# Performance work log

Hardware: AMD Instinct MI355X
Metric: run time of the kernel (lower is better)

Reference implementation:

```python
import jax, jax.numpy as jnp
import numpy as np


def conv1d(x, w, b, pad):
    # x: (B, Cin, T), w: (Cout, Cin, K), b: (Cout,)
    y = jax.lax.conv_general_dilated(x, w, window_strides=(1,), padding=[(pad, pad)],
                                     dimension_numbers=('NCH', 'OIH', 'NCH'))
    return y + b[None, :, None]


def setup_inputs() -> dict:
    key = jax.random.key(0)
    ks = jax.random.split(key, 12)
    B, Cm, T1, Ct, T2, Ca = 8, 80, 800, 512, 200, 80
    queries = jax.random.normal(ks[0], (B, Cm, T1), dtype=jnp.float32)
    keys = jax.random.normal(ks[1], (B, Ct, T2), dtype=jnp.float32)
    query_lens = jnp.full((B,), T1, dtype=jnp.int32)
    key_lens = jax.random.randint(ks[2], (B,), T2 // 2, T2 + 1)
    # mask True where key position is padding (>= key_len): (B, T2, 1)
    mask = (jnp.arange(T2)[None, :] >= key_lens[:, None])[:, :, None]
    attn_prior = jax.random.uniform(ks[3], (B, T1, T2), dtype=jnp.float32) + 0.1
    # key_proj: Conv1d(512->1024, k=3, pad=1) + ReLU + Conv1d(1024->80, k=1)
    kp_w1 = jax.random.normal(ks[4], (2 * Ct, Ct, 3), jnp.float32) * 0.02
    kp_b1 = jnp.zeros((2 * Ct,), jnp.float32)
    kp_w2 = jax.random.normal(ks[5], (Ca, 2 * Ct, 1), jnp.float32) * 0.02
    kp_b2 = jnp.zeros((Ca,), jnp.float32)
    # query_proj (3xconv): Conv1d(80->160,k3)+ReLU+Conv1d(160->80,k1)+ReLU+Conv1d(80->80,k1)
    qp_w1 = jax.random.normal(ks[6], (2 * Cm, Cm, 3), jnp.float32) * 0.05
    qp_b1 = jnp.zeros((2 * Cm,), jnp.float32)
    qp_w2 = jax.random.normal(ks[7], (Cm, 2 * Cm, 1), jnp.float32) * 0.05
    qp_b2 = jnp.zeros((Cm,), jnp.float32)
    qp_w3 = jax.random.normal(ks[8], (Ca, Cm, 1), jnp.float32) * 0.05
    qp_b3 = jnp.zeros((Ca,), jnp.float32)
    return {"queries": queries, "keys": keys, "query_lens": query_lens, "mask": mask,
            "attn_prior": attn_prior, "kp_w1": kp_w1, "kp_b1": kp_b1, "kp_w2": kp_w2,
            "kp_b2": kp_b2, "qp_w1": qp_w1, "qp_b1": qp_b1, "qp_w2": qp_w2,
            "qp_b2": qp_b2, "qp_w3": qp_w3, "qp_b3": qp_b3}


def reference(queries, keys, query_lens, mask, attn_prior,
              kp_w1, kp_b1, kp_w2, kp_b2,
              qp_w1, qp_b1, qp_w2, qp_b2, qp_w3, qp_b3):
    # key projection: (B, Ct, T2) -> (B, Ca, T2)
    ke = conv1d(keys, kp_w1, kp_b1, pad=1)
    ke = jax.nn.relu(ke)
    ke = conv1d(ke, kp_w2, kp_b2, pad=0)
    # query projection ('3xconv'): (B, Cm, T1) -> (B, Ca, T1)
    qe = conv1d(queries, qp_w1, qp_b1, pad=1)
    qe = jax.nn.relu(qe)
    qe = conv1d(qe, qp_w2, qp_b2, pad=0)
    qe = jax.nn.relu(qe)
    qe = conv1d(qe, qp_w3, qp_b3, pad=0)
    # broadcasted squared L2 distance: (B, Ca, T1, T2) -> reduce C -> (B, 1, T1, T2)
    diff2 = (qe[:, :, :, None] - ke[:, :, None, :]) ** 2
    attn = -0.0005 * jnp.sum(diff2, axis=1, keepdims=True)
    # prior in log domain
    attn = jax.nn.log_softmax(attn, axis=3) + jnp.log(attn_prior[:, None] + 1e-8)
    attn_logprob = attn
    # mask (B, T2, 1) -> (B, 1, 1, T2)
    m = jnp.transpose(mask, (0, 2, 1))[:, :, None, :]
    attn = jnp.where(m, -jnp.inf, attn)
    attn = jax.nn.softmax(attn, axis=3)
    return (attn, attn_logprob)
```

## Files before the change

### kernel.cpp

```cpp
#include <hip/hip_runtime.h>
#include <hip/hip_bf16.h>
#include <math.h>

#define B_  8
#define CM  80
#define T1_ 800
#define CT  512
#define T2_ 200
#define CA  80

using bf16 = __hip_bfloat16;
typedef __attribute__((ext_vector_type(8))) short bf16x8;
typedef __attribute__((ext_vector_type(4))) float f32x4;

#define LDSW 56
#define LDSW2 72
#define LDSW3 168
#define LDSW4 104

__device__ __forceinline__ float load_sel(const void* p, long idx, int isf32) {
  if (isf32) return ((const float*)p)[idx];
  return __bfloat162float(((const bf16*)p)[idx]);
}

__device__ __forceinline__ unsigned short f2bf(float x) {
  bf16 h = __float2bfloat16(x);
  return *reinterpret_cast<unsigned short*>(&h);
}

__device__ __forceinline__ int detect_f32(const unsigned short* q) {
  __shared__ int s_f;
  const int tid = threadIdx.x;
  if (tid < 64) {
    unsigned short u = q[2 * tid];
    int e = (u >> 7) & 0xFF;
    unsigned long long bal = __ballot(e < 100 || e > 154);
    if (tid == 0) s_f = (__popcll(bal) >= 16) ? 1 : 0;
  }
  __syncthreads();
  return s_f;
}

__device__ void task_cvt_t(const void* X, bf16* XT, int f, int C, int T,
                           int id2, int tilesT, float* smem, int tid) {
  const int per_b = tilesT * ((C + 31) >> 5);
  const int b = id2 / per_b;
  const int r = id2 - b * per_b;
  const int ct = r / tilesT, tt = r - ct * tilesT;
  const int c0 = ct * 32, t0 = tt * 32;
  const int tx = tid & 31, trow = tid >> 5;
#pragma unroll
  for (int p = 0; p < 4; ++p) {
    const int cr = trow + 8 * p;
    if (c0 + cr < C && t0 + tx < T)
      smem[cr * 33 + tx] = load_sel(X, ((long)b * C + c0 + cr) * T + t0 + tx, f);
  }
  __syncthreads();
#pragma unroll
  for (int p = 0; p < 4; ++p) {
    const int tr = trow + 8 * p;
    if (t0 + tr < T && c0 + tx < C)
      XT[((long)b * T + t0 + tr) * C + c0 + tx] =
          __float2bfloat16(smem[tx * 33 + tr]);
  }
}

__device__ void task_wt3v(const void* W, bf16* WT, int f, int Co, int Ci,
                          int id2, int tid) {
  const int i = id2 * 256 + tid;
  const int g4 = Ci >> 2;
  if (i >= Co * g4) return;
  const int co = i / g4, ci = (i - co * g4) * 4;
  const long sbase = ((long)co * Ci + ci) * 3;
  float w[12];
  if (f) {
    const float4* s = (const float4*)((const float*)W + sbase);
    float4 f0 = s[0], f1 = s[1], f2 = s[2];
    w[0]=f0.x; w[1]=f0.y; w[2]=f0.z; w[3]=f0.w; w[4]=f1.x; w[5]=f1.y;
    w[6]=f1.z; w[7]=f1.w; w[8]=f2.x; w[9]=f2.y; w[10]=f2.z; w[11]=f2.w;
  } else {
#pragma unroll
    for (int j = 0; j < 12; ++j) w[j] = load_sel(W, sbase + j, 0);
  }
#pragma unroll
  for (int dk = 0; dk < 3; ++dk) {
    ushort4 u;
    u.x = f2bf(w[0 * 3 + dk]); u.y = f2bf(w[1 * 3 + dk]);
    u.z = f2bf(w[2 * 3 + dk]); u.w = f2bf(w[3 * 3 + dk]);
    *(ushort4*)(WT + ((long)dk * Co + co) * Ci + ci) = u;
  }
}

__device__ void task_cvtv(const void* W, bf16* O, int f, int n, int id2, int tid) {
  const int i = (id2 * 256 + tid) * 4;
  if (i >= n) return;
  ushort4 u;
  if (f) {
    float4 v = *(const float4*)((const float*)W + i);
    u.x = f2bf(v.x); u.y = f2bf(v.y); u.z = f2bf(v.z); u.w = f2bf(v.w);
  } else {
    u.x = f2bf(load_sel(W, i, 0));     u.y = f2bf(load_sel(W, i + 1, 0));
    u.z = f2bf(load_sel(W, i + 2, 0)); u.w = f2bf(load_sel(W, i + 3, 0));
  }
  *(ushort4*)(O + i) = u;
}

__global__ __launch_bounds__(256) void k_prep(
    const void* __restrict__ queries, const void* __restrict__ keys,
    const void* __restrict__ mask,
    const void* __restrict__ kp_w1, const void* __restrict__ kp_b1,
    const void* __restrict__ kp_w2, const void* __restrict__ kp_b2,
    const void* __restrict__ qp_w1, const void* __restrict__ qp_b1,
    const void* __restrict__ qp_w2, const void* __restrict__ qp_b2,
    const void* __restrict__ qp_w3, const void* __restrict__ qp_b3,
    bf16* __restrict__ keysT, bf16* __restrict__ queriesT,
    bf16* __restrict__ w1T, bf16* __restrict__ qw1T,
    bf16* __restrict__ kw2c, bf16* __restrict__ qw2c, bf16* __restrict__ qw3c,
    float* __restrict__ biasf, float* __restrict__ mf, float* __restrict__ kn) {
  __shared__ float smem[32 * 33];
  const int tid = threadIdx.x;
  const int f = detect_f32((const unsigned short*)queries);
  int id = blockIdx.x;

  if (id < 896) { task_cvt_t(keys, keysT, f, CT, T2_, id, 7, smem, tid); return; }
  id -= 896;
  if (id < 600) { task_cvt_t(queries, queriesT, f, CM, T1_, id, 25, smem, tid); return; }
  id -= 600;
  if (id < 512) { task_wt3v(kp_w1, w1T, f, 1024, CT, id, tid); return; }
  id -= 512;
  if (id < 13) { task_wt3v(qp_w1, qw1T, f, 160, CM, id, tid); return; }
  id -= 13;
  if (id < 80) { task_cvtv(kp_w2, kw2c, f, 80 * 1024, id, tid); return; }
  id -= 80;
  if (id < 13) { task_cvtv(qp_w2, qw2c, f, 80 * 160, id, tid); return; }
  id -= 13;
  if (id < 7) { task_cvtv(qp_w3, qw3c, f, 80 * 80, id, tid); return; }
  id -= 7;

  if (id == 0) {
    for (int i = tid; i < 1424; i += 256) {
      float v;
      if (i < 1024)      v = load_sel(kp_b1, i, f);
      else if (i < 1104) v = load_sel(kp_b2, i - 1024, f);
      else if (i < 1264) v = load_sel(qp_b1, i - 1104, f);
      else if (i < 1344) v = load_sel(qp_b2, i - 1264, f);
      else               v = load_sel(qp_b3, i - 1344, f);
      biasf[i] = v;
    }
    for (int i = tid; i < B_ * T2_; i += 256) kn[i] = 0.f;
    return;
  }

  {
    int* s_fmt = (int*)smem;
    const int nmask = B_ * T2_;
    if (tid == 0) s_fmt[0] = 1;
    __syncthreads();
    const unsigned int* wi = (const unsigned int*)mask;
    const int nw = nmask / 4;
    int pri = 0;
    for (int i = tid; i < nw; i += 256) {
      unsigned int w = wi[i];
      if (w == 0u || w == 1u) continue;
      if (w == 0x3F803F80u || w == 0x00003F80u) { pri = max(pri, 2); continue; }
      if (w == 0x3F800000u) continue;
      unsigned int b0 = w & 0xFFu, b1 = (w >> 8) & 0xFFu,
                   b2 = (w >> 16) & 0xFFu, b3 = (w >> 24) & 0xFFu;
      if (b0 <= 1u && b1 <= 1u && b2 <= 1u && b3 <= 1u) pri = max(pri, 3);
      else pri = max(pri, 2);
    }
    if (pri) atomicMax(&s_fmt[0], pri);
    __syncthreads();
    const int fmt = s_fmt[0];
    for (int i = tid; i < nmask; i += 256) {
      int m;
      if (fmt == 3)      m = ((const unsigned char*)mask)[i] != 0;
      else if (fmt == 2) m = ((const unsigned short*)mask)[i] != 0;
      else               m = (wi[i] != 0u);
      mf[i] = (float)m;
    }
  }
}

__device__ void conv_tile(
    const bf16* __restrict__ XT, const bf16* __restrict__ WT,
    const float* __restrict__ bias, void* __restrict__ Y,
    int Cin, int Cout, int T, int KW, int pad, int relu, int outmode,
    int m0, int n0, short* As, short* Bs, float* Y2 = nullptr) {
  const int K = Cin * KW;
  const int tid = threadIdx.x;
  const int wave = tid >> 6;
  const int lane = tid & 63;

  const int row = tid >> 2;
  const int koff = (tid & 3) * 8;
  const int n = n0 + row;
  const int bb = n / T;
  const int t = n - bb * T;

  const int wm = (wave >> 1) * 32;
  const int wn = (wave & 1) * 32;
  const int fm = lane & 15;
  const int quad = lane >> 4;

  f32x4 acc[2][2] = {};

  const short* ap0 = As + (wm + fm) * LDSW + quad * 8;
  const short* bp0 = Bs + (wn + fm) * LDSW + quad * 8;

  for (int k0 = 0; k0 < K; k0 += 32) {
    {
      const int k = k0 + koff;
      const int m = m0 + row;
      uint4 v = {0u, 0u, 0u, 0u};
      if (m < Cout && k < K) {
        const int dk = k / Cin;
        const int ci = k - dk * Cin;
        v = *(const uint4*)(WT + ((long)dk * Cout + m) * Cin + ci);
      }
      *(uint4*)(As + row * LDSW + koff) = v;
    }
    {
      const int k = k0 + koff;
      uint4 v = {0u, 0u, 0u, 0u};
      if (k < K) {
        const int dk = k / Cin;
        const int ci = k - dk * Cin;
        const int tt = t + dk - pad;
        if (tt >= 0 && tt < T)
          v = *(const uint4*)(XT + ((long)bb * T + tt) * Cin + ci);
      }
      *(uint4*)(Bs + row * LDSW + koff) = v;
    }
    __syncthreads();
    {
      bf16x8 a0 = *(const bf16x8*)(ap0);
      bf16x8 a1 = *(const bf16x8*)(ap0 + 16 * LDSW);
      bf16x8 b0 = *(const bf16x8*)(bp0);
      bf16x8 b1 = *(const bf16x8*)(bp0 + 16 * LDSW);
      acc[0][0] = __builtin_amdgcn_mfma_f32_16x16x32_bf16(a0, b0, acc[0][0], 0, 0, 0);
      acc[0][1] = __builtin_amdgcn_mfma_f32_16x16x32_bf16(a0, b1, acc[0][1], 0, 0, 0);
      acc[1][0] = __builtin_amdgcn_mfma_f32_16x16x32_bf16(a1, b0, acc[1][0], 0, 0, 0);
      acc[1][1] = __builtin_amdgcn_mfma_f32_16x16x32_bf16(a1, b1, acc[1][1], 0, 0, 0);
    }
    __syncthreads();
  }

#pragma unroll
  for (int mi = 0; mi < 2; ++mi) {
    const int mrow = m0 + wm + mi * 16 + quad * 4;
    if (mrow >= Cout) continue;
    float bi[4];
#pragma unroll
    for (int r = 0; r < 4; ++r) bi[r] = bias[mrow + r];
#pragma unroll
    for (int ni = 0; ni < 2; ++ni) {
      const int ncol = n0 + wn + ni * 16 + fm;
      float o[4];
#pragma unroll
      for (int r = 0; r < 4; ++r) {
        float v = acc[mi][ni][r] + bi[r];
        if (relu) v = fmaxf(v, 0.f);
        o[r] = v;
      }
      if (outmode == 0) {
        ushort4 u;
        u.x = f2bf(o[0]); u.y = f2bf(o[1]); u.z = f2bf(o[2]); u.w = f2bf(o[3]);
        *(ushort4*)((bf16*)Y + (long)ncol * Cout + mrow) = u;
      } else if (outmode == 1) {
        *(float4*)((float*)Y + (long)ncol * Cout + mrow) =
            make_float4(o[0], o[1], o[2], o[3]);
      } else {
        const int bb2 = ncol / T;
        const int tloc = ncol - bb2 * T;
        float s4 = 0.f;
#pragma unroll
        for (int r = 0; r < 4; ++r) {
          ((float*)Y)[((long)bb2 * Cout + mrow + r) * T + tloc] = -2.f * o[r];
          s4 = fmaf(o[r], o[r], s4);
        }
        atomicAdd(&Y2[ncol], s4);
      }
    }
  }
}

__device__ void conv_tile128(
    const bf16* __restrict__ XT, const bf16* __restrict__ WT,
    const float* __restrict__ bias, bf16* __restrict__ Y,
    int m0, int n0, short* As, short* Bs) {
  const int Cin = CT, Cout = 1024, T = T2_, K = 1536;
  const int tid = threadIdx.x;
  const int wave = tid >> 6;
  const int lane = tid & 63;

  const int rowb = tid >> 2;
  const int nb = n0 + rowb;
  const int bbb = nb / T;
  const int tb = nb - bbb * T;

  const int wm = (wave >> 1) * 64;
  const int wn = (wave & 1) * 32;
  const int fm = lane & 15;
  const int quad = lane >> 4;

  f32x4 acc[4][2] = {};

  const short* ap0 = As + (wm + fm) * LDSW2 + quad * 8;
  const short* bp0 = Bs + (wn + fm) * LDSW2 + quad * 8;

  for (int k0 = 0; k0 < K; k0 += 64) {
    const int dk = k0 >> 9;
    const int ci0 = k0 & 511;
    {
      const int arow = tid >> 1;
      const bf16* src = WT + ((long)dk * Cout + m0 + arow) * Cin + ci0 + (tid & 1) * 32;
      short* dst = As + arow * LDSW2 + (tid & 1) * 32;
#pragma unroll
      for (int hh = 0; hh < 4; ++hh)
        *(uint4*)(dst + hh * 8) = *(const uint4*)(src + hh * 8);
    }
    {
      const int tt = tb + dk - 1;
      const int kc0 = (tid & 3) * 16;
      if (tt >= 0 && tt < T) {
        const bf16* src = XT + ((long)bbb * T + tt) * Cin + ci0 + kc0;
        short* dst = Bs + rowb * LDSW2 + kc0;
        *(uint4*)(dst) = *(const uint4*)(src);
        *(uint4*)(dst + 8) = *(const uint4*)(src + 8);
      } else {
        uint4 z = {0u, 0u, 0u, 0u};
        short* dst = Bs + rowb * LDSW2 + kc0;
        *(uint4*)(dst) = z;
        *(uint4*)(dst + 8) = z;
      }
    }
    __syncthreads();
#pragma unroll
    for (int h = 0; h < 2; ++h) {
      bf16x8 b0 = *(const bf16x8*)(bp0 + h * 32);
      bf16x8 b1 = *(const bf16x8*)(bp0 + 16 * LDSW2 + h * 32);
#pragma unroll
      for (int mi = 0; mi < 4; ++mi) {
        bf16x8 a = *(const bf16x8*)(ap0 + mi * 16 * LDSW2 + h * 32);
        acc[mi][0] = __builtin_amdgcn_mfma_f32_16x16x32_bf16(a, b0, acc[mi][0], 0, 0, 0);
        acc[mi][1] = __builtin_amdgcn_mfma_f32_16x16x32_bf16(a, b1, acc[mi][1], 0, 0, 0);
      }
    }
    __syncthreads();
  }

#pragma unroll
  for (int mi = 0; mi < 4; ++mi) {
    const int mrow = m0 + wm + mi * 16 + quad * 4;
    float bi[4];
#pragma unroll
    for (int r = 0; r < 4; ++r) bi[r] = bias[mrow + r];
#pragma unroll
    for (int ni = 0; ni < 2; ++ni) {
      const int ncol = n0 + wn + ni * 16 + fm;
      const long base = (long)ncol * Cout + mrow;
      ushort4 u;
      u.x = f2bf(fmaxf(acc[mi][ni][0] + bi[0], 0.f));
      u.y = f2bf(fmaxf(acc[mi][ni][1] + bi[1], 0.f));
      u.z = f2bf(fmaxf(acc[mi][ni][2] + bi[2], 0.f));
      u.w = f2bf(fmaxf(acc[mi][ni][3] + bi[3], 0.f));
      *(ushort4*)(Y + base) = u;
    }
  }
}

__global__ __launch_bounds__(256) void k_conv1(
    const bf16* __restrict__ keysT, const bf16* __restrict__ w1T,
    const float* __restrict__ b_k1, bf16* __restrict__ ke1T,
    const bf16* __restrict__ queriesT, const bf16* __restrict__ qw1T,
    const float* __restrict__ b_q1, bf16* __restrict__ qe1T) {
  __shared__ __align__(16) short sA[128 * LDSW2];
  __shared__ __align__(16) short sB[64 * LDSW2];
  int j = blockIdx.x;
  if (j < 200) {
    conv_tile128(keysT, w1T, b_k1, ke1T, (j / 25) * 128, (j % 25) * 64, sA, sB);
  } else {
    j -= 200;
    conv_tile(queriesT, qw1T, b_q1, qe1T, CM, 160, T1_, 3, 1, 1, 0,
              (j / 100) * 64, (j % 100) * 64, sA, sA + 64 * LDSW);
  }
}

__device__ void conv23_tile(
    const bf16* __restrict__ qe1T, const bf16* __restrict__ qw2c,
    const float* __restrict__ b_q2, const bf16* __restrict__ qw3c,
    const float* __restrict__ b_q3, float* __restrict__ qeT,
    float* __restrict__ qn, int n0, short* smem) {
  short* sIn = smem;
  short* sW2 = smem + 64 * LDSW3;
  short* sC  = smem;
  short* sW3 = smem + 64 * LDSW3;
  const int tid = threadIdx.x;
  const int wave = tid >> 6;
  const int lane = tid & 63;
  const int fm = lane & 15;
  const int quad = lane >> 4;

#pragma unroll
  for (int c = tid; c < 1280; c += 256) {
    const int row = c / 20, kc = (c - row * 20) * 8;
    uint4 v = *(const uint4*)(qe1T + (long)(n0 + row) * 160 + kc);
    *(uint4*)(sIn + row * LDSW3 + kc) = v;
  }
  for (int c = tid; c < 1600; c += 256) {
    const int row = c / 20, kc = (c - row * 20) * 8;
    uint4 v = *(const uint4*)(qw2c + (long)row * 160 + kc);
    *(uint4*)(sW2 + row * LDSW3 + kc) = v;
  }
  __syncthreads();

  f32x4 acc1[5] = {};
#pragma unroll
  for (int ks = 0; ks < 5; ++ks) {
    bf16x8 b = *(const bf16x8*)(sIn + (16 * wave + fm) * LDSW3 + ks * 32 + quad * 8);
#pragma unroll
    for (int mt = 0; mt < 5; ++mt) {
      bf16x8 a = *(const bf16x8*)(sW2 + (16 * mt + fm) * LDSW3 + ks * 32 + quad * 8);
      acc1[mt] = __builtin_amdgcn_mfma_f32_16x16x32_bf16(a, b, acc1[mt], 0, 0, 0);
    }
  }
  __syncthreads();

#pragma unroll
  for (int mt = 0; mt < 5; ++mt) {
    const int ch = 16 * mt + quad * 4;
    const float4 b2 = *(const float4*)(b_q2 + ch);
    ushort4 u;
    u.x = f2bf(fmaxf(acc1[mt][0] + b2.x, 0.f));
    u.y = f2bf(fmaxf(acc1[mt][1] + b2.y, 0.f));
    u.z = f2bf(fmaxf(acc1[mt][2] + b2.z, 0.f));
    u.w = f2bf(fmaxf(acc1[mt][3] + b2.w, 0.f));
    *(ushort4*)(sC + (16 * wave + fm) * LDSW4 + ch) = u;
  }
  if (tid < 128) {
    const int row = tid >> 1, off = 80 + (tid & 1) * 8;
    uint4 z = {0u, 0u, 0u, 0u};
    *(uint4*)(sC + row * LDSW4 + off) = z;
  }
  for (int c = tid; c < 800; c += 256) {
    const int row = c / 10, kc = (c - row * 10) * 8;
    uint4 v = *(const uint4*)(qw3c + (long)row * 80 + kc);
    *(uint4*)(sW3 + row * LDSW4 + kc) = v;
  }
  if (tid < 160) {
    const int row = tid >> 1, off = 80 + (tid & 1) * 8;
    uint4 z = {0u, 0u, 0u, 0u};
    *(uint4*)(sW3 + row * LDSW4 + off) = z;
  }
  __syncthreads();

  f32x4 acc2[5] = {};
#pragma unroll
  for (int ks = 0; ks < 3; ++ks) {
    bf16x8 b = *(const bf16x8*)(sC + (16 * wave + fm) * LDSW4 + ks * 32 + quad * 8);
#pragma unroll
    for (int mt = 0; mt < 5; ++mt) {
      bf16x8 a = *(const bf16x8*)(sW3 + (16 * mt + fm) * LDSW4 + ks * 32 + quad * 8);
      acc2[mt] = __builtin_amdgcn_mfma_f32_16x16x32_bf16(a, b, acc2[mt], 0, 0, 0);
    }
  }

  const int pos = n0 + 16 * wave + fm;
  float p = 0.f;
#pragma unroll
  for (int mt = 0; mt < 5; ++mt) {
    const int ch = 16 * mt + quad * 4;
    const float4 b3 = *(const float4*)(b_q3 + ch);
    float4 o = make_float4(acc2[mt][0] + b3.x, acc2[mt][1] + b3.y,
                           acc2[mt][2] + b3.z, acc2[mt][3] + b3.w);
    p = fmaf(o.x, o.x, p); p = fmaf(o.y, o.y, p);
    p = fmaf(o.z, o.z, p); p = fmaf(o.w, o.w, p);
    *(float4*)(qeT + (long)pos * CA + ch) = o;
  }
  p += __shfl_xor(p, 16, 64);
  p += __shfl_xor(p, 32, 64);
  if (quad == 0) qn[pos] = p;
}

__global__ __launch_bounds__(256) void k_conv2f(
    const bf16* __restrict__ ke1T, const bf16* __restrict__ kw2c,
    const float* __restrict__ b_k2, float* __restrict__ keT,
    float* __restrict__ kn,
    const bf16* __restrict__ qe1T, const bf16* __restrict__ qw2c,
    const float* __restrict__ b_q2, const bf16* __restrict__ qw3c,
    const float* __restrict__ b_q3, float* __restrict__ qeT,
    float* __restrict__ qn) {
  __shared__ __align__(16) short smem[64 * LDSW3 + 80 * LDSW3];
  int j = blockIdx.x;
  if (j < 50) {
    conv_tile(ke1T, kw2c, b_k2, keT, 1024, CA, T2_, 1, 0, 0, 2,
              (j / 25) * 64, (j % 25) * 64, smem, smem + 64 * LDSW, kn);
  } else {
    conv23_tile(qe1T, qw2c, b_q2, qw3c, b_q3, qeT, qn, (j - 50) * 64, smem);
  }
}

__global__ __launch_bounds__(256) void k_dist(
    const float* __restrict__ qeT, const float* __restrict__ keT2,
    const float* __restrict__ kn, const float* __restrict__ qn,
    const void* __restrict__ prior, const float* __restrict__ mf,
    void* __restrict__ out, const unsigned short* __restrict__ qprobe) {
  __shared__ float sq[4 * CA];
  __shared__ float sqn[4];
  __shared__ float redA[16], redB[16], redC[16], redD[16];
  const int f = detect_f32(qprobe);
  const int b = blockIdx.y;
  const int t1base = blockIdx.x * 4;
  const int tid = threadIdx.x;
  const int wid = tid >> 6;

  for (int i = tid; i < 4 * CA; i += 256) {
    int u = i / CA, c = i - u * CA;
    sq[i] = qeT[((long)b * T1_ + t1base + u) * CA + c];
  }
  if (tid < 4) sqn[tid] = qn[b * T1_ + t1base + tid];
  __syncthreads();

  const int t2 = tid;
  const bool valid = (t2 < T2_);
  float x[4] = {-INFINITY, -INFINITY, -INFINITY, -INFINITY};
  if (valid) {
    const float* kp = keT2 + (long)b * CA * T2_ + t2;
    const float knv = kn[b * T2_ + t2];
    float s[4] = {0.f, 0.f, 0.f, 0.f};
#pragma unroll 8
    for (int j = 0; j < CA; ++j) {
      const float kv = kp[j * T2_];
      s[0] = fmaf(kv, sq[0 * CA + j], s[0]);
      s[1] = fmaf(kv, sq[1 * CA + j], s[1]);
      s[2] = fmaf(kv, sq[2 * CA + j], s[2]);
      s[3] = fmaf(kv, sq[3 * CA + j], s[3]);
    }
#pragma unroll
    for (int u = 0; u < 4; ++u)
      x[u] = -0.0005f * (s[u] + sqn[u] + knv);
  }

  const float mval = valid ? mf[b * T2_ + t2] : 0.f;
  const long N = (long)B_ * T1_ * T2_;

  float m[4] = {x[0], x[1], x[2], x[3]};
#pragma unroll
  for (int o = 32; o > 0; o >>= 1)
#pragma unroll
    for (int u = 0; u < 4; ++u) m[u] = fmaxf(m[u], __shfl_down(m[u], o, 64));
  if ((tid & 63) == 0)
#pragma unroll
    for (int u = 0; u < 4; ++u) redA[wid * 4 + u] = m[u];
  __syncthreads();
  float M1[4];
#pragma unroll
  for (int u = 0; u < 4; ++u)
    M1[u] = fmaxf(fmaxf(redA[u], redA[4 + u]), fmaxf(redA[8 + u], redA[12 + u]));

  float e[4], s1[4];
#pragma unroll
  for (int u = 0; u < 4; ++u) {
    e[u] = (x[u] == -INFINITY) ? 0.f : expf(x[u] - M1[u]);
    s1[u] = e[u];
  }
#pragma unroll
  for (int o = 32; o > 0; o >>= 1)
#pragma unroll
    for (int u = 0; u < 4; ++u) s1[u] += __shfl_down(s1[u], o, 64);
  if ((tid & 63) == 0)
#pragma unroll
    for (int u = 0; u < 4; ++u) redB[wid * 4 + u] = s1[u];
  __syncthreads();
  float lp[4];
#pragma unroll
  for (int u = 0; u < 4; ++u) {
    const float S1 = redB[u] + redB[4 + u] + redB[8 + u] + redB[12 + u];
    const float logZ = logf(S1);
    lp[u] = -INFINITY;
    if (valid) {
      const long oidx = ((long)b * T1_ + t1base + u) * T2_ + t2;
      float pr = load_sel(prior, oidx, f);
      lp[u] = (x[u] - M1[u] - logZ) + logf(fmaxf(pr, 0.f) + 1e-8f);
      if (f) ((float*)out)[N + oidx] = lp[u];
      else   ((bf16*)out)[N + oidx] = __float2bfloat16(lp[u]);
    }
  }

  float xm[4], m2[4];
#pragma unroll
  for (int u = 0; u < 4; ++u) {
    xm[u] = (valid && mval != 0.f) ? -INFINITY : lp[u];
    m2[u] = xm[u];
  }
#pragma unroll
  for (int o = 32; o > 0; o >>= 1)
#pragma unroll
    for (int u = 0; u < 4; ++u) m2[u] = fmaxf(m2[u], __shfl_down(m2[u], o, 64));
  if ((tid & 63) == 0)
#pragma unroll
    for (int u = 0; u < 4; ++u) redC[wid * 4 + u] = m2[u];
  __syncthreads();
  float M2[4];
#pragma unroll
  for (int u = 0; u < 4; ++u)
    M2[u] = fmaxf(fmaxf(redC[u], redC[4 + u]), fmaxf(redC[8 + u], redC[12 + u]));

  float e2[4], s2[4];
#pragma unroll
  for (int u = 0; u < 4; ++u) {
    e2[u] = (xm[u] == -INFINITY) ? 0.f : expf(xm[u] - M2[u]);
    s2[u] = e2[u];
  }
#pragma unroll
  for (int o = 32; o > 0; o >>= 1)
#pragma unroll
    for (int u = 0; u < 4; ++u) s2[u] += __shfl_down(s2[u], o, 64);
  if ((tid & 63) == 0)
#pragma unroll
    for (int u = 0; u < 4; ++u) redD[wid * 4 + u] = s2[u];
  __syncthreads();
#pragma unroll
  for (int u = 0; u < 4; ++u) {
    const float S2 = redD[u] + redD[4 + u] + redD[8 + u] + redD[12 + u];
    if (valid) {
      float a = (S2 > 0.f) ? (e2[u] / S2) : 0.f;
      const long oidx = ((long)b * T1_ + t1base + u) * T2_ + t2;
      if (f) ((float*)out)[oidx] = a;
      else   ((bf16*)out)[oidx] = __float2bfloat16(a);
    }
  }
}

extern "C" void kernel_launch(void* const* d_in, const int* in_sizes, int n_in,
                              void* d_out, int out_size, void* d_ws, size_t ws_size,
                              hipStream_t stream) {
  const void* queries = d_in[0];
  const void* keys    = d_in[1];
  const void* mask    = d_in[3];
  const void* prior   = d_in[4];
  const void* kp_w1 = d_in[5];
  const void* kp_b1 = d_in[6];
  const void* kp_w2 = d_in[7];
  const void* kp_b2 = d_in[8];
  const void* qp_w1 = d_in[9];
  const void* qp_b1 = d_in[10];
  const void* qp_w2 = d_in[11];
  const void* qp_b2 = d_in[12];
  const void* qp_w3 = d_in[13];
  const void* qp_b3 = d_in[14];

  float* keT   = (float*)d_ws;
  float* qeT   = keT + 128000;
  float* mf    = qeT + 512000;
  float* biasf = mf + 1600;
  float* kn    = biasf + 1440;
  float* qn    = kn + 1600;
  bf16* keysT    = (bf16*)(qn + 6400);
  bf16* queriesT = keysT + 819200;
  bf16* w1T      = queriesT + 512000;
  bf16* qw1T     = w1T + 1572864;
  bf16* kw2c     = qw1T + 38400;
  bf16* qw2c     = kw2c + 81920;
  bf16* qw3c     = qw2c + 12800;
  bf16* ke1T     = qw3c + 6400;
  bf16* qe1T     = ke1T + 1638400;

  float* b_k1 = biasf;
  float* b_k2 = biasf + 1024;
  float* b_q1 = biasf + 1104;
  float* b_q2 = biasf + 1264;
  float* b_q3 = biasf + 1344;

  k_prep<<<2123, 256, 0, stream>>>(
      queries, keys, mask,
      kp_w1, kp_b1, kp_w2, kp_b2,
      qp_w1, qp_b1, qp_w2, qp_b2, qp_w3, qp_b3,
      keysT, queriesT, w1T, qw1T, kw2c, qw2c, qw3c, biasf, mf, kn);

  k_conv1<<<500, 256, 0, stream>>>(keysT, w1T, b_k1, ke1T,
                                   queriesT, qw1T, b_q1, qe1T);

  k_conv2f<<<150, 256, 0, stream>>>(ke1T, kw2c, b_k2, keT, kn,
                                    qe1T, qw2c, b_q2, qw3c, b_q3, qeT, qn);

  k_dist<<<dim3(200, B_), 256, 0, stream>>>(
      qeT, keT, kn, qn, prior, mf, d_out, (const unsigned short*)queries);
}
```

Before: 168.4 us.

## Prefetch next K-tile into registers in conv GEMMs, vectorize distance loop, use fast math

Both conv GEMM kernels now issue the global loads for the next K-slice into registers before the barrier and MFMA work of the current slice. This overlaps global memory latency with compute. The attention kernel's dot-product loop reads the query rows from LDS as float4 and unrolls by four channels. expf/logf are swapped for the __expf/__logf intrinsics, which are faster but slightly less accurate.

```diff
diff --git a/kernel.cpp b/kernel.cpp
--- a/kernel.cpp
+++ b/kernel.cpp
@@ -208,29 +208,39 @@
   const short* ap0 = As + (wm + fm) * LDSW + quad * 8;
   const short* bp0 = Bs + (wn + fm) * LDSW + quad * 8;
 
+  auto loadA = [&](int k0) -> uint4 {
+    const int k = k0 + koff;
+    const int m = m0 + row;
+    uint4 v = {0u, 0u, 0u, 0u};
+    if (m < Cout && k < K) {
+      const int dk = k / Cin;
+      const int ci = k - dk * Cin;
+      v = *(const uint4*)(WT + ((long)dk * Cout + m) * Cin + ci);
+    }
+    return v;
+  };
+  auto loadB = [&](int k0) -> uint4 {
+    const int k = k0 + koff;
+    uint4 v = {0u, 0u, 0u, 0u};
+    if (k < K) {
+      const int dk = k / Cin;
+      const int ci = k - dk * Cin;
+      const int tt = t + dk - pad;
+      if (tt >= 0 && tt < T)
+        v = *(const uint4*)(XT + ((long)bb * T + tt) * Cin + ci);
+    }
+    return v;
+  };
+
+  uint4 va = loadA(0);
+  uint4 vb = loadB(0);
+
   for (int k0 = 0; k0 < K; k0 += 32) {
-    {
-      const int k = k0 + koff;
-      const int m = m0 + row;
-      uint4 v = {0u, 0u, 0u, 0u};
-      if (m < Cout && k < K) {
-        const int dk = k / Cin;
-        const int ci = k - dk * Cin;
-        v = *(const uint4*)(WT + ((long)dk * Cout + m) * Cin + ci);
-      }
-      *(uint4*)(As + row * LDSW + koff) = v;
-    }
-    {
-      const int k = k0 + koff;
-      uint4 v = {0u, 0u, 0u, 0u};
-      if (k < K) {
-        const int dk = k / Cin;
-        const int ci = k - dk * Cin;
-        const int tt = t + dk - pad;
-        if (tt >= 0 && tt < T)
-          v = *(const uint4*)(XT + ((long)bb * T + tt) * Cin + ci);
-      }
-      *(uint4*)(Bs + row * LDSW + koff) = v;
+    *(uint4*)(As + row * LDSW + koff) = va;
+    *(uint4*)(Bs + row * LDSW + koff) = vb;
+    if (k0 + 32 < K) {
+      va = loadA(k0 + 32);
+      vb = loadB(k0 + 32);
     }
     __syncthreads();
     {
@@ -309,31 +319,49 @@
   const short* ap0 = As + (wm + fm) * LDSW2 + quad * 8;
   const short* bp0 = Bs + (wn + fm) * LDSW2 + quad * 8;
 
-  for (int k0 = 0; k0 < K; k0 += 64) {
+  const int arow = tid >> 1;
+  const int acol = (tid & 1) * 32;
+  const int kcb = (tid & 3) * 16;
+
+  uint4 va[4];
+  uint4 vb0, vb1;
+
+  auto loadA = [&](int k0) {
     const int dk = k0 >> 9;
     const int ci0 = k0 & 511;
+    const bf16* src = WT + ((long)dk * Cout + m0 + arow) * Cin + ci0 + acol;
+#pragma unroll
+    for (int hh = 0; hh < 4; ++hh) va[hh] = *(const uint4*)(src + hh * 8);
+  };
+  auto loadB = [&](int k0) {
+    const int dk = k0 >> 9;
+    const int ci0 = k0 & 511;
+    const int tt = tb + dk - 1;
+    if (tt >= 0 && tt < T) {
+      const bf16* src = XT + ((long)bbb * T + tt) * Cin + ci0 + kcb;
+      vb0 = *(const uint4*)(src);
+      vb1 = *(const uint4*)(src + 8);
+    } else {
+      uint4 z = {0u, 0u, 0u, 0u};
+      vb0 = z; vb1 = z;
+    }
+  };
+
+  loadA(0);
+  loadB(0);
+
+  for (int k0 = 0; k0 < K; k0 += 64) {
     {
-      const int arow = tid >> 1;
-      const bf16* src = WT + ((long)dk * Cout + m0 + arow) * Cin + ci0 + (tid & 1) * 32;
-      short* dst = As + arow * LDSW2 + (tid & 1) * 32;
-#pragma unroll
-      for (int hh = 0; hh < 4; ++hh)
-        *(uint4*)(dst + hh * 8) = *(const uint4*)(src + hh * 8);
-    }
-    {
-      const int tt = tb + dk - 1;
-      const int kc0 = (tid & 3) * 16;
-      if (tt >= 0 && tt < T) {
-        const bf16* src = XT + ((long)bbb * T + tt) * Cin + ci0 + kc0;
-        short* dst = Bs + rowb * LDSW2 + kc0;
-        *(uint4*)(dst) = *(const uint4*)(src);
-        *(uint4*)(dst + 8) = *(const uint4*)(src + 8);
-      } else {
-        uint4 z = {0u, 0u, 0u, 0u};
-        short* dst = Bs + rowb * LDSW2 + kc0;
-        *(uint4*)(dst) = z;
-        *(uint4*)(dst + 8) = z;
-      }
+      short* dst = As + arow * LDSW2 + acol;
+#pragma unroll
+      for (int hh = 0; hh < 4; ++hh) *(uint4*)(dst + hh * 8) = va[hh];
+      short* dstb = Bs + rowb * LDSW2 + kcb;
+      *(uint4*)(dstb) = vb0;
+      *(uint4*)(dstb + 8) = vb1;
+    }
+    if (k0 + 64 < K) {
+      loadA(k0 + 64);
+      loadB(k0 + 64);
     }
     __syncthreads();
 #pragma unroll
@@ -528,18 +556,30 @@
   if (valid) {
     const float* kp = keT2 + (long)b * CA * T2_ + t2;
     const float knv = kn[b * T2_ + t2];
-    float s[4] = {0.f, 0.f, 0.f, 0.f};
-#pragma unroll 8
-    for (int j = 0; j < CA; ++j) {
-      const float kv = kp[j * T2_];
-      s[0] = fmaf(kv, sq[0 * CA + j], s[0]);
-      s[1] = fmaf(kv, sq[1 * CA + j], s[1]);
-      s[2] = fmaf(kv, sq[2 * CA + j], s[2]);
-      s[3] = fmaf(kv, sq[3 * CA + j], s[3]);
-    }
-#pragma unroll
-    for (int u = 0; u < 4; ++u)
-      x[u] = -0.0005f * (s[u] + sqn[u] + knv);
+    float a0 = 0.f, a1 = 0.f, a2 = 0.f, a3 = 0.f;
+#pragma unroll 2
+    for (int j = 0; j < CA; j += 4) {
+      const float4 q0 = *(const float4*)(sq + 0 * CA + j);
+      const float4 q1 = *(const float4*)(sq + 1 * CA + j);
+      const float4 q2 = *(const float4*)(sq + 2 * CA + j);
+      const float4 q3 = *(const float4*)(sq + 3 * CA + j);
+      const float k0v = kp[(j + 0) * T2_];
+      const float k1v = kp[(j + 1) * T2_];
+      const float k2v = kp[(j + 2) * T2_];
+      const float k3v = kp[(j + 3) * T2_];
+      a0 = fmaf(k0v, q0.x, a0); a0 = fmaf(k1v, q0.y, a0);
+      a0 = fmaf(k2v, q0.z, a0); a0 = fmaf(k3v, q0.w, a0);
+      a1 = fmaf(k0v, q1.x, a1); a1 = fmaf(k1v, q1.y, a1);
+      a1 = fmaf(k2v, q1.z, a1); a1 = fmaf(k3v, q1.w, a1);
+      a2 = fmaf(k0v, q2.x, a2); a2 = fmaf(k1v, q2.y, a2);
+      a2 = fmaf(k2v, q2.z, a2); a2 = fmaf(k3v, q2.w, a2);
+      a3 = fmaf(k0v, q3.x, a3); a3 = fmaf(k1v, q3.y, a3);
+      a3 = fmaf(k2v, q3.z, a3); a3 = fmaf(k3v, q3.w, a3);
+    }
+    x[0] = -0.0005f * (a0 + sqn[0] + knv);
+    x[1] = -0.0005f * (a1 + sqn[1] + knv);
+    x[2] = -0.0005f * (a2 + sqn[2] + knv);
+    x[3] = -0.0005f * (a3 + sqn[3] + knv);
   }
 
   const float mval = valid ? mf[b * T2_ + t2] : 0.f;
@@ -562,7 +602,7 @@
   float e[4], s1[4];
 #pragma unroll
   for (int u = 0; u < 4; ++u) {
-    e[u] = (x[u] == -INFINITY) ? 0.f : expf(x[u] - M1[u]);
+    e[u] = (x[u] == -INFINITY) ? 0.f : __expf(x[u] - M1[u]);
     s1[u] = e[u];
   }
 #pragma unroll
@@ -577,12 +617,12 @@
 #pragma unroll
   for (int u = 0; u < 4; ++u) {
     const float S1 = redB[u] + redB[4 + u] + redB[8 + u] + redB[12 + u];
-    const float logZ = logf(S1);
+    const float logZ = __logf(S1);
     lp[u] = -INFINITY;
     if (valid) {
       const long oidx = ((long)b * T1_ + t1base + u) * T2_ + t2;
       float pr = load_sel(prior, oidx, f);
-      lp[u] = (x[u] - M1[u] - logZ) + logf(fmaxf(pr, 0.f) + 1e-8f);
+      lp[u] = (x[u] - M1[u] - logZ) + __logf(fmaxf(pr, 0.f) + 1e-8f);
       if (f) ((float*)out)[N + oidx] = lp[u];
       else   ((bf16*)out)[N + oidx] = __float2bfloat16(lp[u]);
     }
@@ -610,7 +650,7 @@
   float e2[4], s2[4];
 #pragma unroll
   for (int u = 0; u < 4; ++u) {
-    e2[u] = (xm[u] == -INFINITY) ? 0.f : expf(xm[u] - M2[u]);
+    e2[u] = (xm[u] == -INFINITY) ? 0.f : __expf(xm[u] - M2[u]);
     s2[u] = e2[u];
   }
 #pragma unroll
```

Measured after the change: 168.2 us. About the same (-0.2%).
